# Performance work log

Measured on AMD Instinct MI355X. Metric: run time of the kernel, lower is better.

Reference implementation:

```python
import jax, jax.numpy as jnp
import numpy as np
from jax import lax

B, T, H = 4096, 2048, 32


def setup_inputs() -> dict:
    key = jax.random.key(0)
    ks = jax.random.split(key, 10)
    s = 1.0 / np.sqrt(H)  # PyTorch LSTM/Linear init scale
    x = jax.random.normal(ks[0], (B, T, 1), dtype=jnp.float32)
    lengths = jax.random.randint(ks[1], (B,), 1, T + 1, dtype=jnp.int32)
    u = lambda k, shape, sc: jax.random.uniform(k, shape, jnp.float32, -sc, sc)
    return {
        "x": x,
        "lengths": lengths,
        # backward-direction LSTM weights (only h_n[-1] is used by the head)
        "w_ih": u(ks[2], (4 * H, 1), s),
        "w_hh": u(ks[3], (4 * H, H), s),
        "b_ih": u(ks[4], (4 * H,), s),
        "b_hh": u(ks[5], (4 * H,), s),
        "fc_w": u(ks[6], (64, H), 1.0 / np.sqrt(H)),
        "fc_b": u(ks[7], (64,), 1.0 / np.sqrt(H)),
        "fc2_w": u(ks[8], (1, 64), 1.0 / np.sqrt(64)),
        "fc2_b": u(ks[9], (1,), 1.0 / np.sqrt(64)),
    }


def _backward_lstm_final(x, lengths, w_ih, w_hh, b_ih, b_hh):
    """Final hidden state of the backward direction of a packed BiLSTM.

    The backward direction reads each sequence from t=len-1 down to t=0 with
    zero initial state. Equivalently: scan padded x in reverse time order and
    only update (h, c) where t < length (packed-sequence semantics).
    """
    Bv, Tv, _ = x.shape
    ts = jnp.arange(Tv - 1, -1, -1)                       # reversed time indices
    xs_t = jnp.transpose(x[:, ::-1, :], (1, 0, 2))        # [T, B, 1]
    mask_t = ts[:, None] < lengths[None, :]               # [T, B]

    def step(carry, inp):
        h, c = carry
        xt, m = inp                                        # [B,1], [B]
        gates = xt @ w_ih.T + b_ih + h @ w_hh.T + b_hh     # [B, 4H]
        i, f, g, o = jnp.split(gates, 4, axis=-1)
        i = jax.nn.sigmoid(i)
        f = jax.nn.sigmoid(f)
        g = jnp.tanh(g)
        o = jax.nn.sigmoid(o)
        c_new = f * c + i * g
        h_new = o * jnp.tanh(c_new)
        mm = m[:, None]
        return (jnp.where(mm, h_new, h), jnp.where(mm, c_new, c)), None

    h0 = jnp.zeros((Bv, H), dtype=x.dtype)
    c0 = jnp.zeros((Bv, H), dtype=x.dtype)
    (h_n, _), _ = lax.scan(step, (h0, c0), (xs_t, mask_t))
    return h_n                                             # [B, H]


def reference(x, lengths, w_ih, w_hh, b_ih, b_hh, fc_w, fc_b, fc2_w, fc2_b):
    h_n = _backward_lstm_final(x, lengths, w_ih, w_hh, b_ih, b_hh)
    out = jax.nn.elu(h_n @ fc_w.T + fc_b)                  # [B, 64]
    out = jax.nn.sigmoid(out @ fc2_w.T + fc2_b)            # [B, 1]
    return out
```

## Files before the change

### kernel.cpp

```cpp
#include <hip/hip_runtime.h>
#include <hip/hip_bf16.h>

constexpr int BB = 4096;
constexpr int TT = 2048;
constexpr int HH = 32;

typedef float v2f __attribute__((ext_vector_type(2)));
typedef float v4f __attribute__((ext_vector_type(4)));

__device__ __forceinline__ float fexp2(float x) { return __builtin_amdgcn_exp2f(x); }
__device__ __forceinline__ float frcp(float x)  { return __builtin_amdgcn_rcpf(x); }
__device__ __forceinline__ float fsigmoid(float x) {
    return frcp(1.0f + fexp2(x * -1.4426950408889634f));
}
__device__ __forceinline__ float felu(float x) {
    return x > 0.0f ? x : (fexp2(x * 1.4426950408889634f) - 1.0f);
}

__global__ void sort_by_len_kernel(const int* __restrict__ lengths, int* __restrict__ perm) {
    __shared__ int hist[TT];
    __shared__ int csum[256];
    const int tid = threadIdx.x;
    for (int i = tid; i < TT; i += 256) hist[i] = 0;
    __syncthreads();
    for (int i = tid; i < BB; i += 256) atomicAdd(&hist[TT - lengths[i]], 1);
    __syncthreads();
    const int base = tid * 8;
    int loc[8];
    int s = 0;
#pragma unroll
    for (int j = 0; j < 8; ++j) { loc[j] = hist[base + j]; s += loc[j]; }
    csum[tid] = s;
    __syncthreads();
    for (int off = 1; off < 256; off <<= 1) {
        int v = (tid >= off) ? csum[tid - off] : 0;
        __syncthreads();
        csum[tid] += v;
        __syncthreads();
    }
    int run = csum[tid] - s;
#pragma unroll
    for (int j = 0; j < 8; ++j) { int t = loc[j]; hist[base + j] = run; run += t; }
    __syncthreads();
    for (int i = tid; i < BB; i += 256) {
        int pos = atomicAdd(&hist[TT - lengths[i]], 1);
        perm[pos] = i;
    }
}

__global__ __attribute__((amdgpu_flat_work_group_size(64, 64), amdgpu_waves_per_eu(2, 3)))
void lstm_kernel(const float* __restrict__ x, const int* __restrict__ lengths,
                 const float* __restrict__ w_ih, const float* __restrict__ w_hh,
                 const float* __restrict__ b_ih, const float* __restrict__ b_hh,
                 const float* __restrict__ fc_w, const float* __restrict__ fc_b,
                 const float* __restrict__ fc2_w, const float* __restrict__ fc2_b,
                 float* __restrict__ out, const int* __restrict__ perm) {
    __shared__ __align__(16) float hbuf[64];
    __shared__ float xbuf[64];

    const int lane = threadIdx.x;
    const int b = perm ? perm[blockIdx.x] : blockIdx.x;
    const int L = lengths[b];

    const int r0 = lane;
    const int r1 = lane + 64;

    const bool  lower  = lane < 32;
    const float NL2E   = -1.4426950408889634f;
    const float scale0 = NL2E;
    const float scale1 = lower ? 2.0f * NL2E : NL2E;
    const float amul   = lower ? 2.0f : 1.0f;
    const float badd   = lower ? -1.0f : 0.0f;

    v2f w0[16], w1[16];
    {
        const v2f* p0 = reinterpret_cast<const v2f*>(w_hh + r0 * 32);
        const v2f* p1 = reinterpret_cast<const v2f*>(w_hh + r1 * 32);
#pragma unroll
        for (int q = 0; q < 16; ++q) {
            w0[q] = p0[q] * scale0;
            w1[q] = p1[q] * scale1;
        }
    }
    float wi0 = w_ih[r0] * scale0;
    float wi1 = w_ih[r1] * scale1;
    float bi0 = (b_ih[r0] + b_hh[r0]) * scale0;
    float bi1 = (b_ih[r1] + b_hh[r1]) * scale1;

#pragma unroll
    for (int q = 0; q < 16; ++q) {
        asm volatile("" : "+v"(w0[q]), "+v"(w1[q]));
    }
    asm volatile("" : "+v"(wi0), "+v"(wi1), "+v"(bi0), "+v"(bi1));

    v2f h2[16];
#pragma unroll
    for (int q = 0; q < 16; ++q) h2[q] = (v2f){0.0f, 0.0f};
    float c = 0.0f;
    const float* xb = x + (size_t)b * TT;

    int t = L - 1;
    while (t >= 0) {
        const int tb = t & ~63;
        __syncthreads();
        xbuf[lane] = xb[tb + lane];
        __syncthreads();
        for (; t >= tb; --t) {
            const float xt = xbuf[t - tb];
            v2f a0 = (v2f){fmaf(wi0, xt, bi0), 0.0f};
            v2f a1 = (v2f){fmaf(wi1, xt, bi1), 0.0f};
#pragma unroll
            for (int q = 0; q < 16; ++q) {
                a0 = __builtin_elementwise_fma(w0[q], h2[q], a0);
                a1 = __builtin_elementwise_fma(w1[q], h2[q], a1);
            }
            const float g0 = a0.x + a0.y;
            const float g1 = a1.x + a1.y;
            const float s0 = frcp(1.0f + fexp2(g0));
            const float s1 = frcp(1.0f + fexp2(g1));
            const float v1 = fmaf(amul, s1, badd);
            const float fg = __shfl_xor(s0, 32);
            const float og = __shfl_xor(v1, 32);
            c = fmaf(fg, c, s0 * v1);
            const float tc = 1.0f - 2.0f * frcp(1.0f + fexp2(c * 2.8853900817779268f));
            const float hn = og * tc;
            hbuf[lane] = hn;
            __syncthreads();
            const v4f* hp = reinterpret_cast<const v4f*>(hbuf);
#pragma unroll
            for (int q = 0; q < 8; ++q) {
                v4f r = hp[q];
                h2[2 * q]     = r.xy;
                h2[2 * q + 1] = r.zw;
            }
        }
    }

    float a = fc_b[lane];
    {
        const v2f* fp = reinterpret_cast<const v2f*>(fc_w + lane * 32);
        v2f fa = (v2f){0.0f, 0.0f};
#pragma unroll
        for (int q = 0; q < 16; ++q) fa = __builtin_elementwise_fma(fp[q], h2[q], fa);
        a += fa.x + fa.y;
    }
    float partial = felu(a) * fc2_w[lane];
#pragma unroll
    for (int m = 32; m >= 1; m >>= 1) partial += __shfl_xor(partial, m, 64);
    if (lane == 0) out[b] = fsigmoid(partial + fc2_b[0]);
}

extern "C" void kernel_launch(void* const* d_in, const int* in_sizes, int n_in,
                              void* d_out, int out_size, void* d_ws, size_t ws_size,
                              hipStream_t stream) {
    const float* x       = (const float*)d_in[0];
    const int*   lengths = (const int*)d_in[1];
    const float* w_ih    = (const float*)d_in[2];
    const float* w_hh    = (const float*)d_in[3];
    const float* b_ih    = (const float*)d_in[4];
    const float* b_hh    = (const float*)d_in[5];
    const float* fc_w    = (const float*)d_in[6];
    const float* fc_b    = (const float*)d_in[7];
    const float* fc2_w   = (const float*)d_in[8];
    const float* fc2_b   = (const float*)d_in[9];
    float* out = (float*)d_out;

    int* perm = nullptr;
    if (ws_size >= (size_t)BB * sizeof(int)) {
        perm = (int*)d_ws;
        hipLaunchKernelGGL(sort_by_len_kernel, dim3(1), dim3(256), 0, stream, lengths, perm);
    }
    hipLaunchKernelGGL(lstm_kernel, dim3(BB), dim3(64), 0, stream,
                       x, lengths, w_ih, w_hh, b_ih, b_hh,
                       fc_w, fc_b, fc2_w, fc2_b, out, perm);
}
```

Before: 691.2 us.

## Use packed fp16 dot products for LSTM recurrence and drop per-step barriers

The recurrent weights and the hidden state are stored as half precision. The 32-wide matrix-vector product per gate row now uses v_dot2 fp16 instructions with two accumulators, which halves the instruction count and register footprint of the inner step. The cell update is moved to the upper 32 lanes so only one cross-lane shuffle is needed per step. The __syncthreads around the LDS hidden-state exchange are removed because the block is a single wavefront. The costs are reduced precision over 2048 recurrent steps and reliance on in-wave LDS ordering; the waves_per_eu hint is also loosened.

```diff
diff --git a/kernel.cpp b/kernel.cpp
--- a/kernel.cpp
+++ b/kernel.cpp
@@ -7,6 +7,8 @@
 
 typedef float v2f __attribute__((ext_vector_type(2)));
 typedef float v4f __attribute__((ext_vector_type(4)));
+typedef _Float16 v2h __attribute__((ext_vector_type(2)));
+typedef _Float16 v8h __attribute__((ext_vector_type(8)));
 
 __device__ __forceinline__ float fexp2(float x) { return __builtin_amdgcn_exp2f(x); }
 __device__ __forceinline__ float frcp(float x)  { return __builtin_amdgcn_rcpf(x); }
@@ -48,14 +50,14 @@
     }
 }
 
-__global__ __attribute__((amdgpu_flat_work_group_size(64, 64), amdgpu_waves_per_eu(2, 3)))
+__global__ __attribute__((amdgpu_flat_work_group_size(64, 64), amdgpu_waves_per_eu(1, 4)))
 void lstm_kernel(const float* __restrict__ x, const int* __restrict__ lengths,
                  const float* __restrict__ w_ih, const float* __restrict__ w_hh,
                  const float* __restrict__ b_ih, const float* __restrict__ b_hh,
                  const float* __restrict__ fc_w, const float* __restrict__ fc_b,
                  const float* __restrict__ fc2_w, const float* __restrict__ fc2_b,
                  float* __restrict__ out, const int* __restrict__ perm) {
-    __shared__ __align__(16) float hbuf[64];
+    __shared__ __align__(16) _Float16 hs[64];
     __shared__ float xbuf[64];
 
     const int lane = threadIdx.x;
@@ -72,14 +74,15 @@
     const float amul   = lower ? 2.0f : 1.0f;
     const float badd   = lower ? -1.0f : 0.0f;
 
-    v2f w0[16], w1[16];
+    v2h w0[16], w1[16];
     {
         const v2f* p0 = reinterpret_cast<const v2f*>(w_hh + r0 * 32);
         const v2f* p1 = reinterpret_cast<const v2f*>(w_hh + r1 * 32);
 #pragma unroll
         for (int q = 0; q < 16; ++q) {
-            w0[q] = p0[q] * scale0;
-            w1[q] = p1[q] * scale1;
+            v2f a = p0[q]; v2f bq = p1[q];
+            w0[q] = (v2h){(_Float16)(a.x * scale0), (_Float16)(a.y * scale0)};
+            w1[q] = (v2h){(_Float16)(bq.x * scale1), (_Float16)(bq.y * scale1)};
         }
     }
     float wi0 = w_ih[r0] * scale0;
@@ -91,58 +94,73 @@
     for (int q = 0; q < 16; ++q) {
         asm volatile("" : "+v"(w0[q]), "+v"(w1[q]));
     }
-    asm volatile("" : "+v"(wi0), "+v"(wi1), "+v"(bi0), "+v"(bi1));
 
-    v2f h2[16];
+    v8h hr[4];
 #pragma unroll
-    for (int q = 0; q < 16; ++q) h2[q] = (v2f){0.0f, 0.0f};
+    for (int q = 0; q < 4; ++q) hr[q] = (v8h)(_Float16)0.0f;
     float c = 0.0f;
     const float* xb = x + (size_t)b * TT;
 
     int t = L - 1;
     while (t >= 0) {
         const int tb = t & ~63;
-        __syncthreads();
         xbuf[lane] = xb[tb + lane];
-        __syncthreads();
         for (; t >= tb; --t) {
             const float xt = xbuf[t - tb];
-            v2f a0 = (v2f){fmaf(wi0, xt, bi0), 0.0f};
-            v2f a1 = (v2f){fmaf(wi1, xt, bi1), 0.0f};
+            float a0  = fmaf(wi0, xt, bi0);
+            float a1  = fmaf(wi1, xt, bi1);
+            float a0b = 0.0f, a1b = 0.0f;
 #pragma unroll
-            for (int q = 0; q < 16; ++q) {
-                a0 = __builtin_elementwise_fma(w0[q], h2[q], a0);
-                a1 = __builtin_elementwise_fma(w1[q], h2[q], a1);
+            for (int q = 0; q < 4; ++q) {
+                const v8h hh = hr[q];
+                const v2h p01 = __builtin_shufflevector(hh, hh, 0, 1);
+                const v2h p23 = __builtin_shufflevector(hh, hh, 2, 3);
+                const v2h p45 = __builtin_shufflevector(hh, hh, 4, 5);
+                const v2h p67 = __builtin_shufflevector(hh, hh, 6, 7);
+                a0  = __builtin_amdgcn_fdot2(w0[4*q+0], p01, a0,  false);
+                a0b = __builtin_amdgcn_fdot2(w0[4*q+1], p23, a0b, false);
+                a0  = __builtin_amdgcn_fdot2(w0[4*q+2], p45, a0,  false);
+                a0b = __builtin_amdgcn_fdot2(w0[4*q+3], p67, a0b, false);
+                a1  = __builtin_amdgcn_fdot2(w1[4*q+0], p01, a1,  false);
+                a1b = __builtin_amdgcn_fdot2(w1[4*q+1], p23, a1b, false);
+                a1  = __builtin_amdgcn_fdot2(w1[4*q+2], p45, a1,  false);
+                a1b = __builtin_amdgcn_fdot2(w1[4*q+3], p67, a1b, false);
             }
-            const float g0 = a0.x + a0.y;
-            const float g1 = a1.x + a1.y;
+            const float g0 = a0 + a0b;
+            const float g1 = a1 + a1b;
             const float s0 = frcp(1.0f + fexp2(g0));
             const float s1 = frcp(1.0f + fexp2(g1));
             const float v1 = fmaf(amul, s1, badd);
-            const float fg = __shfl_xor(s0, 32);
-            const float og = __shfl_xor(v1, 32);
-            c = fmaf(fg, c, s0 * v1);
+            const float ig = s0 * v1;
+            const float igx = __shfl_xor(ig, 32);
+            c = fmaf(s0, c, igx);
             const float tc = 1.0f - 2.0f * frcp(1.0f + fexp2(c * 2.8853900817779268f));
-            const float hn = og * tc;
-            hbuf[lane] = hn;
-            __syncthreads();
-            const v4f* hp = reinterpret_cast<const v4f*>(hbuf);
+            const float hn = v1 * tc;
+            hs[lane] = (_Float16)hn;
+            const v8h* hp = reinterpret_cast<const v8h*>(hs + 32);
 #pragma unroll
-            for (int q = 0; q < 8; ++q) {
-                v4f r = hp[q];
-                h2[2 * q]     = r.xy;
-                h2[2 * q + 1] = r.zw;
-            }
+            for (int q = 0; q < 4; ++q) hr[q] = hp[q];
         }
     }
 
+    float hf[32];
+#pragma unroll
+    for (int q = 0; q < 4; ++q) {
+        const v8h hh = hr[q];
+#pragma unroll
+        for (int j = 0; j < 8; ++j) hf[8 * q + j] = (float)hh[j];
+    }
     float a = fc_b[lane];
     {
-        const v2f* fp = reinterpret_cast<const v2f*>(fc_w + lane * 32);
-        v2f fa = (v2f){0.0f, 0.0f};
+        const v4f* fp = reinterpret_cast<const v4f*>(fc_w + lane * 32);
 #pragma unroll
-        for (int q = 0; q < 16; ++q) fa = __builtin_elementwise_fma(fp[q], h2[q], fa);
-        a += fa.x + fa.y;
+        for (int q = 0; q < 8; ++q) {
+            const v4f f = fp[q];
+            a = fmaf(f.x, hf[4 * q + 0], a);
+            a = fmaf(f.y, hf[4 * q + 1], a);
+            a = fmaf(f.z, hf[4 * q + 2], a);
+            a = fmaf(f.w, hf[4 * q + 3], a);
+        }
     }
     float partial = felu(a) * fc2_w[lane];
 #pragma unroll
```

New measurement: 643.8 us. -6.9%, faster.
